# Optimization experiments

Measured on AMD Instinct MI355X. Metric: run time of the kernel, lower is better.

Reference implementation:

```python
import jax, jax.numpy as jnp
import numpy as np

B, S, D, H = 2, 2048, 1024, 16
HD = D // H  # head_dim = 64

def setup_inputs() -> dict:
    key = jax.random.key(0)
    ks = jax.random.split(key, 5)
    scale = 1.0 / np.sqrt(D)
    x = jax.random.normal(ks[0], (B, S, D), dtype=jnp.float32)
    Wq = jax.random.normal(ks[1], (D, D), dtype=jnp.float32) * scale
    Wk = jax.random.normal(ks[2], (D, D), dtype=jnp.float32) * scale
    Wv = jax.random.normal(ks[3], (D, D), dtype=jnp.float32) * scale
    Wf = jax.random.normal(ks[4], (D, D), dtype=jnp.float32) * scale
    z = jnp.zeros((D,), dtype=jnp.float32)
    return {"x": x, "Wq": Wq, "bq": z, "Wk": Wk, "bk": z, "Wv": Wv, "bv": z, "Wf": Wf, "bf": z}

def reference(x, Wq, bq, Wk, bk, Wv, bv, Wf, bf):
    # Linear layers follow torch convention: y = x @ W.T + b
    def split_heads(t):  # [B,S,D] -> [B,H,S,HD]
        return t.reshape(B, S, H, HD).transpose(0, 2, 1, 3)
    q = split_heads(x @ Wq.T + bq)
    k = split_heads(x @ Wk.T + bk)
    v = split_heads(x @ Wv.T + bv)
    scores = jnp.einsum('bhqd,bhkd->bhqk', q, k) / jnp.sqrt(jnp.float32(HD))
    causal = jnp.tril(jnp.ones((S, S), dtype=bool))  # [S,S]
    scores = jnp.where(causal[None, None], scores, -jnp.inf)
    attn = jax.nn.softmax(scores, axis=-1)
    out = jnp.einsum('bhqk,bhkd->bhqd', attn, v)
    out = out.transpose(0, 2, 1, 3).reshape(B, S, D)
    return out @ Wf.T + bf
```

## Files before the change

kernel.cpp:

```cpp
#include <hip/hip_runtime.h>
#include <stdint.h>

#define B_  2
#define S_  2048
#define D_  1024
#define H_  16
#define HD_ 64
#define M_  (B_*S_)

typedef __bf16 bf16x8 __attribute__((ext_vector_type(8)));
typedef float  f32x4  __attribute__((ext_vector_type(4)));

typedef const __attribute__((address_space(1))) void* gas_ptr;
typedef __attribute__((address_space(3))) void* las_ptr;

__device__ __forceinline__ uint16_t f32_to_bf16(float f) {
  uint32_t u = __float_as_uint(f);
  u += 0x7FFFu + ((u >> 16) & 1u);
  return (uint16_t)(u >> 16);
}

__device__ __forceinline__ uint16_t f32_to_bf16_rtz(float f) {
  return (uint16_t)(__float_as_uint(f) >> 16);
}

__device__ __forceinline__ void g2l16(const uint16_t* g, uint16_t* l) {
  __builtin_amdgcn_global_load_lds((gas_ptr)g, (las_ptr)l, 16, 0, 0);
}

__device__ __forceinline__ int swz_src(int s) {
  return (s >> 2) * D_ + (((s & 3) ^ ((s >> 3) & 3)) * 8);
}

__global__ void cast_all(const float* __restrict__ x,
                         const float* __restrict__ wq, const float* __restrict__ wk,
                         const float* __restrict__ wv, const float* __restrict__ wf,
                         uint16_t* __restrict__ xb,
                         uint16_t* __restrict__ wqb, uint16_t* __restrict__ wkb,
                         uint16_t* __restrict__ wvb, uint16_t* __restrict__ wfb) {
  const int X4 = M_ * D_ / 4;
  const int W4 = D_ * D_ / 4;
  int i = blockIdx.x * 256 + threadIdx.x;
  const float* src; uint16_t* dst; int off;
  if (i < X4) { src = x; dst = xb; off = i; }
  else {
    int j = i - X4;
    int w = j >> 18;
    off = j & (W4 - 1);
    src = (w == 0) ? wq : (w == 1) ? wk : (w == 2) ? wv : wf;
    dst = (w == 0) ? wqb : (w == 1) ? wkb : (w == 2) ? wvb : wfb;
  }
  float4 v = ((const float4*)src)[off];
  ushort4 o;
  o.x = f32_to_bf16(v.x); o.y = f32_to_bf16(v.y);
  o.z = f32_to_bf16(v.z); o.w = f32_to_bf16(v.w);
  ((ushort4*)dst)[off] = o;
}

__global__ __launch_bounds__(512, 2)
void qkv_gemm(const uint16_t* __restrict__ xb,
              const uint16_t* __restrict__ wqb, const uint16_t* __restrict__ wkb,
              const uint16_t* __restrict__ wvb,
              const float* __restrict__ bqv, const float* __restrict__ bkv,
              const float* __restrict__ bvv,
              uint16_t* __restrict__ qout, uint16_t* __restrict__ kout,
              uint16_t* __restrict__ vtout)
{
  __shared__ __align__(16) uint16_t As[2][2][8192];
  __shared__ __align__(16) uint16_t Bs[2][2][8192];

  const int wsel = blockIdx.x >> 2;
  const int nsel = blockIdx.x & 3;
  const int mtile = blockIdx.y;
  const int tid  = threadIdx.x;
  const int lane = tid & 63, wave = tid >> 6;
  const int quad = lane >> 4, l16 = lane & 15;
  const int wm = (wave >> 2) * 128;
  const int wn = (wave & 3) * 64;
  const int sw = quad ^ ((l16 >> 1) & 3);

  const uint16_t *Ap, *Bp;
  int m0e, n0e;
  if (wsel < 2) {
    Ap = xb; Bp = (wsel == 0) ? wqb : wkb;
    m0e = mtile * 256; n0e = nsel * 256;
  } else {
    Ap = wvb; Bp = xb;
    m0e = nsel * 256; n0e = mtile * 256;
  }

  const int so0 = swz_src(tid);
  const int so1 = swz_src(tid + 512);
  const uint16_t* gA = Ap + (size_t)m0e * D_;
  const uint16_t* gB = Bp + (size_t)n0e * D_;
  const int d0 = (wave * 64) * 8;
  const int d1 = (512 + wave * 64) * 8;

  f32x4 acc[8][4];
  #pragma unroll
  for (int i = 0; i < 8; ++i)
    #pragma unroll
    for (int j = 0; j < 4; ++j)
      #pragma unroll
      for (int e = 0; e < 4; ++e)
        acc[i][j][e] = 0.f;

  g2l16(gA + so0,      &As[0][0][d0]);
  g2l16(gA + 32 + so0, &As[0][1][d0]);
  g2l16(gB + so0,      &Bs[0][0][d0]);
  g2l16(gB + 32 + so0, &Bs[0][1][d0]);
  g2l16(gA + so1,      &As[0][0][d1]);
  g2l16(gA + 32 + so1, &As[0][1][d1]);
  g2l16(gB + so1,      &Bs[0][0][d1]);
  g2l16(gB + 32 + so1, &Bs[0][1][d1]);
  __syncthreads();

  bf16x8 bfr[4][2], afr[2][2];
  for (int t = 0; t < 16; ++t) {
    const int c = t & 1, cn = c ^ 1;
    const bool pf = (t < 15);
    const int kn = (t + 1) * 64;

    #pragma unroll
    for (int nt = 0; nt < 4; ++nt) {
      const int ro = ((wn + nt * 16 + l16) * 4 + sw) * 8;
      bfr[nt][0] = *(const bf16x8*)(&Bs[c][0][ro]);
      bfr[nt][1] = *(const bf16x8*)(&Bs[c][1][ro]);
    }

    #pragma unroll
    for (int p = 0; p < 4; ++p) {
      #pragma unroll
      for (int i = 0; i < 2; ++i) {
        const int ro = ((wm + (2 * p + i) * 16 + l16) * 4 + sw) * 8;
        afr[i][0] = *(const bf16x8*)(&As[c][0][ro]);
        afr[i][1] = *(const bf16x8*)(&As[c][1][ro]);
      }
      if (p == 0 && pf) {
        g2l16(gA + kn + so0,      &As[cn][0][d0]);
        g2l16(gA + kn + 32 + so0, &As[cn][1][d0]);
        g2l16(gB + kn + so0,      &Bs[cn][0][d0]);
        g2l16(gB + kn + 32 + so0, &Bs[cn][1][d0]);
      }
      if (p == 1 && pf) {
        g2l16(gA + kn + so1,      &As[cn][0][d1]);
        g2l16(gA + kn + 32 + so1, &As[cn][1][d1]);
        g2l16(gB + kn + so1,      &Bs[cn][0][d1]);
        g2l16(gB + kn + 32 + so1, &Bs[cn][1][d1]);
      }
      __builtin_amdgcn_s_barrier();
      asm volatile("s_waitcnt lgkmcnt(0)" ::: "memory");
      __builtin_amdgcn_sched_barrier(0);
      __builtin_amdgcn_s_setprio(1);
      #pragma unroll
      for (int i = 0; i < 2; ++i)
        #pragma unroll
        for (int nt = 0; nt < 4; ++nt) {
          acc[2 * p + i][nt] = __builtin_amdgcn_mfma_f32_16x16x32_bf16(
              afr[i][0], bfr[nt][0], acc[2 * p + i][nt], 0, 0, 0);
          acc[2 * p + i][nt] = __builtin_amdgcn_mfma_f32_16x16x32_bf16(
              afr[i][1], bfr[nt][1], acc[2 * p + i][nt], 0, 0, 0);
        }
      __builtin_amdgcn_s_setprio(0);
      if (p == 3) {
        asm volatile("s_waitcnt vmcnt(0)" ::: "memory");
      }
      __builtin_amdgcn_s_barrier();
    }
  }

  if (wsel < 2) {
    const float* bias = (wsel == 0) ? bqv : bkv;
    uint16_t* outp = (wsel == 0) ? qout : kout;
    const float scl = (wsel == 0) ? 0.18033688f : 1.0f;
    #pragma unroll
    for (int nt = 0; nt < 4; ++nt) {
      const int n = n0e + wn + nt * 16 + l16;
      const int h = n >> 6, hd = n & 63;
      const float bia = bias[n];
      #pragma unroll
      for (int mt = 0; mt < 8; ++mt) {
        #pragma unroll
        for (int r = 0; r < 4; ++r) {
          const int m = m0e + wm + mt * 16 + quad * 4 + r;
          const int bb = m >> 11, s = m & (S_ - 1);
          outp[(((size_t)(bb * H_ + h)) * S_ + s) * HD_ + hd] =
              f32_to_bf16((acc[mt][nt][r] + bia) * scl);
        }
      }
    }
  } else {
    #pragma unroll
    for (int mt = 0; mt < 8; ++mt) {
      #pragma unroll
      for (int r = 0; r < 4; ++r) {
        const int m = m0e + wm + mt * 16 + quad * 4 + r;
        const int h = m >> 6, hd = m & 63;
        const float bia = bvv[m];
        #pragma unroll
        for (int nt = 0; nt < 4; ++nt) {
          const int n = n0e + wn + nt * 16 + l16;
          const int bb = n >> 11, s = n & (S_ - 1);
          vtout[(((size_t)(bb * H_ + h)) * HD_ + hd) * S_ + s] =
              f32_to_bf16(acc[mt][nt][r] + bia);
        }
      }
    }
  }
}

__global__ __launch_bounds__(256)
void flash_attn(const uint16_t* __restrict__ qb, const uint16_t* __restrict__ kb,
                const uint16_t* __restrict__ vtb, uint16_t* __restrict__ ao)
{
  __shared__ __align__(16) uint16_t ks[2][64 * 32];
  __shared__ __align__(16) uint16_t vs[2][64 * 32];
  __shared__ __align__(16) uint16_t p_lds[4][16][72];

  const int bh = blockIdx.x;
  const int qt = (int)(gridDim.y - 1u - blockIdx.y);
  const int wave = threadIdx.x >> 6, lane = threadIdx.x & 63;
  const int quad = lane >> 4, l16 = lane & 15;
  const int sw = quad ^ ((l16 >> 1) & 3);
  const int q0 = qt * 64;

  const uint16_t* Q  = qb  + (size_t)bh * S_ * HD_;
  const uint16_t* Kp = kb  + (size_t)bh * S_ * HD_;
  const uint16_t* Vt = vtb + (size_t)bh * HD_ * S_;

  const int qrow = q0 + wave * 16;
  bf16x8 aq0 = *(const bf16x8*)(Q + (size_t)(qrow + l16) * HD_ + quad * 8);
  bf16x8 aq1 = *(const bf16x8*)(Q + (size_t)(qrow + l16) * HD_ + 32 + quad * 8);

  const int srow = lane >> 2;
  const int schk = (lane & 3) ^ ((lane >> 3) & 3);
  const uint16_t* sb[4]; uint16_t* sdst[4]; int sstep[4];
  #pragma unroll
  for (int j = 0; j < 4; ++j) {
    const int g = wave * 4 + j;
    if (g < 8) {
      const int c = (g >> 2) & 1, rb = g & 3;
      sdst[j] = &ks[c][rb * 512];
      sb[j] = Kp + (size_t)(rb * 16 + srow) * HD_ + c * 32 + schk * 8;
      sstep[j] = 64 * HD_;
    } else {
      const int gg = g - 8, c = (gg >> 2) & 1, rb = gg & 3;
      sdst[j] = &vs[c][rb * 512];
      sb[j] = Vt + (size_t)(rb * 16 + srow) * S_ + c * 32 + schk * 8;
      sstep[j] = 64;
    }
  }

  float lpart[4];
  f32x4 o[4];
  #pragma unroll
  for (int r = 0; r < 4; ++r) lpart[r] = 0.f;
  #pragma unroll
  for (int t = 0; t < 4; ++t)
    #pragma unroll
    for (int e = 0; e < 4; ++e) o[t][e] = 0.f;

  const int rowid = qrow + quad * 4;

  for (int kt = 0; kt <= qt; ++kt) {
    const int kbase = kt * 64;
    const bool diag = (kt == qt);

    #pragma unroll
    for (int j = 0; j < 4; ++j) {
      g2l16(sb[j], sdst[j]);
      sb[j] += sstep[j];
    }
    __syncthreads();

    bf16x8 kf0[4], kf1[4];
    #pragma unroll
    for (int nt = 0; nt < 4; ++nt) {
      kf0[nt] = *(const bf16x8*)(&ks[0][((nt * 16 + l16) * 4 + sw) * 8]);
      kf1[nt] = *(const bf16x8*)(&ks[1][((nt * 16 + l16) * 4 + sw) * 8]);
    }
    f32x4 sacc[4];
    #pragma unroll
    for (int nt = 0; nt < 4; ++nt) {
      #pragma unroll
      for (int e = 0; e < 4; ++e) sacc[nt][e] = 0.f;
      sacc[nt] = __builtin_amdgcn_mfma_f32_16x16x32_bf16(aq0, kf0[nt], sacc[nt], 0, 0, 0);
      sacc[nt] = __builtin_amdgcn_mfma_f32_16x16x32_bf16(aq1, kf1[nt], sacc[nt], 0, 0, 0);
    }

    bf16x8 vf0[4], vf1[4];
    #pragma unroll
    for (int t = 0; t < 4; ++t) {
      vf0[t] = *(const bf16x8*)(&vs[0][((t * 16 + l16) * 4 + sw) * 8]);
      vf1[t] = *(const bf16x8*)(&vs[1][((t * 16 + l16) * 4 + sw) * 8]);
    }

    #pragma unroll
    for (int nt = 0; nt < 4; ++nt) {
      const int kkc = kbase + nt * 16 + l16;
      #pragma unroll
      for (int r = 0; r < 4; ++r) {
        float p = __builtin_amdgcn_exp2f(sacc[nt][r]);
        if (diag && (kkc > rowid + r)) p = 0.f;
        lpart[r] += p;
        p_lds[wave][quad * 4 + r][nt * 16 + l16] = f32_to_bf16_rtz(p);
      }
    }

    bf16x8 ap0 = *(const bf16x8*)(&p_lds[wave][l16][quad * 8]);
    bf16x8 ap1 = *(const bf16x8*)(&p_lds[wave][l16][32 + quad * 8]);
    #pragma unroll
    for (int t = 0; t < 4; ++t) {
      o[t] = __builtin_amdgcn_mfma_f32_16x16x32_bf16(ap0, vf0[t], o[t], 0, 0, 0);
      o[t] = __builtin_amdgcn_mfma_f32_16x16x32_bf16(ap1, vf1[t], o[t], 0, 0, 0);
    }
    __syncthreads();
  }

  #pragma unroll
  for (int r = 0; r < 4; ++r) {
    lpart[r] += __shfl_xor(lpart[r], 1, 64);
    lpart[r] += __shfl_xor(lpart[r], 2, 64);
    lpart[r] += __shfl_xor(lpart[r], 4, 64);
    lpart[r] += __shfl_xor(lpart[r], 8, 64);
  }
  const int bb = bh >> 4, h = bh & 15;
  #pragma unroll
  for (int t = 0; t < 4; ++t) {
    #pragma unroll
    for (int r = 0; r < 4; ++r) {
      const float ov = o[t][r] / lpart[r];
      ao[((size_t)(bb * S_ + rowid + r)) * D_ + h * HD_ + t * 16 + l16] =
          f32_to_bf16(ov);
    }
  }
}

__global__ __launch_bounds__(256)
void out_gemm(const uint16_t* __restrict__ ab, const uint16_t* __restrict__ wfb,
              const float* __restrict__ bfv, float* __restrict__ out)
{
  __shared__ __align__(16) uint16_t As[2 * 64 * 32];
  __shared__ __align__(16) uint16_t Bs[2 * 128 * 32];
  const int m0 = blockIdx.y * 64;
  const int n0 = blockIdx.x * 128;
  const int lane = threadIdx.x & 63, wave = threadIdx.x >> 6;
  const int quad = lane >> 4, l16 = lane & 15;
  const int wm = (wave >> 1) * 32, wn = (wave & 1) * 64;
  const int sw = quad ^ ((l16 >> 1) & 3);

  f32x4 acc[2][4];
  #pragma unroll
  for (int i = 0; i < 2; ++i)
    #pragma unroll
    for (int j = 0; j < 4; ++j)
      #pragma unroll
      for (int e = 0; e < 4; ++e)
        acc[i][j][e] = 0.f;

  const int sA  = wave * 64 + lane;
  const int sB1 = sA + 256;
  const int soA = swz_src(sA), soB1 = swz_src(sB1);
  uint16_t* lA  = As + (size_t)(wave * 64) * 8;
  uint16_t* lB0 = Bs + (size_t)(wave * 64) * 8;
  uint16_t* lB1 = Bs + (size_t)(256 + wave * 64) * 8;
  const uint16_t* gA  = ab  + (size_t)m0 * D_ + soA;
  const uint16_t* gB0 = wfb + (size_t)n0 * D_ + soA;
  const uint16_t* gB1 = wfb + (size_t)n0 * D_ + soB1;

  for (int k0 = 0; k0 < D_; k0 += 64) {
    g2l16(gA  + k0,      lA);
    g2l16(gB0 + k0,      lB0);
    g2l16(gB1 + k0,      lB1);
    g2l16(gA  + k0 + 32, lA  + 2048);
    g2l16(gB0 + k0 + 32, lB0 + 4096);
    g2l16(gB1 + k0 + 32, lB1 + 4096);
    __syncthreads();
    bf16x8 af0[2], af1[2], bf0[4], bf1[4];
    #pragma unroll
    for (int mt = 0; mt < 2; ++mt) {
      const int ro = ((wm + mt * 16 + l16) * 4 + sw) * 8;
      af0[mt] = *(const bf16x8*)(As + ro);
      af1[mt] = *(const bf16x8*)(As + 2048 + ro);
    }
    #pragma unroll
    for (int nt = 0; nt < 4; ++nt) {
      const int ro = ((wn + nt * 16 + l16) * 4 + sw) * 8;
      bf0[nt] = *(const bf16x8*)(Bs + ro);
      bf1[nt] = *(const bf16x8*)(Bs + 4096 + ro);
    }
    #pragma unroll
    for (int mt = 0; mt < 2; ++mt)
      #pragma unroll
      for (int nt = 0; nt < 4; ++nt) {
        acc[mt][nt] = __builtin_amdgcn_mfma_f32_16x16x32_bf16(
            af0[mt], bf0[nt], acc[mt][nt], 0, 0, 0);
        acc[mt][nt] = __builtin_amdgcn_mfma_f32_16x16x32_bf16(
            af1[mt], bf1[nt], acc[mt][nt], 0, 0, 0);
      }
    __syncthreads();
  }

  #pragma unroll
  for (int nt = 0; nt < 4; ++nt) {
    const int n = n0 + wn + nt * 16 + l16;
    const float bia = bfv[n];
    #pragma unroll
    for (int mt = 0; mt < 2; ++mt) {
      #pragma unroll
      for (int r = 0; r < 4; ++r) {
        const int m = m0 + wm + mt * 16 + quad * 4 + r;
        out[(size_t)m * D_ + n] = acc[mt][nt][r] + bia;
      }
    }
  }
}

extern "C" void kernel_launch(void* const* d_in, const int* in_sizes, int n_in,
                              void* d_out, int out_size, void* d_ws, size_t ws_size,
                              hipStream_t stream) {
  (void)in_sizes; (void)n_in; (void)out_size; (void)ws_size;
  const float* x  = (const float*)d_in[0];
  const float* Wq = (const float*)d_in[1];
  const float* bq = (const float*)d_in[2];
  const float* Wk = (const float*)d_in[3];
  const float* bk = (const float*)d_in[4];
  const float* Wv = (const float*)d_in[5];
  const float* bv = (const float*)d_in[6];
  const float* Wf = (const float*)d_in[7];
  const float* bf = (const float*)d_in[8];
  float* out = (float*)d_out;

  uint16_t* ws = (uint16_t*)d_ws;
  uint16_t* xb   = ws;
  uint16_t* wqb  = xb  + (size_t)M_ * D_;
  uint16_t* wkb  = wqb + (size_t)D_ * D_;
  uint16_t* wvb  = wkb + (size_t)D_ * D_;
  uint16_t* wfb  = wvb + (size_t)D_ * D_;
  uint16_t* qbuf = wfb + (size_t)D_ * D_;
  uint16_t* kbuf = qbuf + (size_t)M_ * D_;
  uint16_t* vtb  = kbuf + (size_t)M_ * D_;
  uint16_t* aob  = vtb  + (size_t)M_ * D_;

  const int CAST_BLOCKS = (M_ * D_ / 4 + 4 * (D_ * D_ / 4)) / 256;
  cast_all<<<CAST_BLOCKS, 256, 0, stream>>>(x, Wq, Wk, Wv, Wf,
                                            xb, wqb, wkb, wvb, wfb);

  qkv_gemm<<<dim3(12, 16), 512, 0, stream>>>(xb, wqb, wkb, wvb, bq, bk, bv,
                                             qbuf, kbuf, vtb);
  flash_attn<<<dim3(32, 32), 256, 0, stream>>>(qbuf, kbuf, vtb, aob);
  out_gemm<<<dim3(8, 64), 256, 0, stream>>>(aob, wfb, bf, out);
}
```

Before: 181.4 us.

## Double-buffer K/V tiles in flash attention and split GEMM k-halves with partial waits

The flash attention kernel now keeps two K/V LDS buffers and prefetches the next key tile while computing the current one, so the global-to-LDS load and barrier no longer sit at the start of each iteration. MFMA blocks are wrapped in s_setprio. The projection GEMM restructures its inner loop by k-half, issuing each half's prefetch and using vmcnt partial waits so compute can start once the first half has landed. This doubles flash-attention LDS usage, which may reduce occupancy, and adds more barriers in the GEMM loop.

```diff
diff --git a/kernel.cpp b/kernel.cpp
--- a/kernel.cpp
+++ b/kernel.cpp
@@ -106,64 +106,73 @@
         acc[i][j][e] = 0.f;
 
   g2l16(gA + so0,      &As[0][0][d0]);
+  g2l16(gA + so1,      &As[0][0][d1]);
+  g2l16(gB + so0,      &Bs[0][0][d0]);
+  g2l16(gB + so1,      &Bs[0][0][d1]);
   g2l16(gA + 32 + so0, &As[0][1][d0]);
-  g2l16(gB + so0,      &Bs[0][0][d0]);
+  g2l16(gA + 32 + so1, &As[0][1][d1]);
   g2l16(gB + 32 + so0, &Bs[0][1][d0]);
-  g2l16(gA + so1,      &As[0][0][d1]);
-  g2l16(gA + 32 + so1, &As[0][1][d1]);
-  g2l16(gB + so1,      &Bs[0][0][d1]);
   g2l16(gB + 32 + so1, &Bs[0][1][d1]);
-  __syncthreads();
-
-  bf16x8 bfr[4][2], afr[2][2];
+  asm volatile("s_waitcnt vmcnt(4)" ::: "memory");
+  __builtin_amdgcn_s_barrier();
+
+  bf16x8 bfr[4], afr[4];
   for (int t = 0; t < 16; ++t) {
     const int c = t & 1, cn = c ^ 1;
     const bool pf = (t < 15);
     const int kn = (t + 1) * 64;
-
-    #pragma unroll
-    for (int nt = 0; nt < 4; ++nt) {
-      const int ro = ((wn + nt * 16 + l16) * 4 + sw) * 8;
-      bfr[nt][0] = *(const bf16x8*)(&Bs[c][0][ro]);
-      bfr[nt][1] = *(const bf16x8*)(&Bs[c][1][ro]);
-    }
-
-    #pragma unroll
-    for (int p = 0; p < 4; ++p) {
-      #pragma unroll
-      for (int i = 0; i < 2; ++i) {
-        const int ro = ((wm + (2 * p + i) * 16 + l16) * 4 + sw) * 8;
-        afr[i][0] = *(const bf16x8*)(&As[c][0][ro]);
-        afr[i][1] = *(const bf16x8*)(&As[c][1][ro]);
-      }
-      if (p == 0 && pf) {
-        g2l16(gA + kn + so0,      &As[cn][0][d0]);
-        g2l16(gA + kn + 32 + so0, &As[cn][1][d0]);
-        g2l16(gB + kn + so0,      &Bs[cn][0][d0]);
-        g2l16(gB + kn + 32 + so0, &Bs[cn][1][d0]);
-      }
-      if (p == 1 && pf) {
-        g2l16(gA + kn + so1,      &As[cn][0][d1]);
-        g2l16(gA + kn + 32 + so1, &As[cn][1][d1]);
-        g2l16(gB + kn + so1,      &Bs[cn][0][d1]);
-        g2l16(gB + kn + 32 + so1, &Bs[cn][1][d1]);
+    #pragma unroll
+    for (int h = 0; h < 2; ++h) {
+      #pragma unroll
+      for (int nt = 0; nt < 4; ++nt) {
+        const int ro = ((wn + nt * 16 + l16) * 4 + sw) * 8;
+        bfr[nt] = *(const bf16x8*)(&Bs[c][h][ro]);
+      }
+      #pragma unroll
+      for (int i = 0; i < 4; ++i) {
+        const int ro = ((wm + i * 16 + l16) * 4 + sw) * 8;
+        afr[i] = *(const bf16x8*)(&As[c][h][ro]);
+      }
+      if (pf) {
+        g2l16(gA + kn + h * 32 + so0, &As[cn][h][d0]);
+        g2l16(gA + kn + h * 32 + so1, &As[cn][h][d1]);
+        g2l16(gB + kn + h * 32 + so0, &Bs[cn][h][d0]);
+        g2l16(gB + kn + h * 32 + so1, &Bs[cn][h][d1]);
       }
       __builtin_amdgcn_s_barrier();
       asm volatile("s_waitcnt lgkmcnt(0)" ::: "memory");
       __builtin_amdgcn_sched_barrier(0);
       __builtin_amdgcn_s_setprio(1);
       #pragma unroll
-      for (int i = 0; i < 2; ++i)
+      for (int i = 0; i < 4; ++i)
         #pragma unroll
-        for (int nt = 0; nt < 4; ++nt) {
-          acc[2 * p + i][nt] = __builtin_amdgcn_mfma_f32_16x16x32_bf16(
-              afr[i][0], bfr[nt][0], acc[2 * p + i][nt], 0, 0, 0);
-          acc[2 * p + i][nt] = __builtin_amdgcn_mfma_f32_16x16x32_bf16(
-              afr[i][1], bfr[nt][1], acc[2 * p + i][nt], 0, 0, 0);
-        }
+        for (int nt = 0; nt < 4; ++nt)
+          acc[i][nt] = __builtin_amdgcn_mfma_f32_16x16x32_bf16(
+              afr[i], bfr[nt], acc[i][nt], 0, 0, 0);
       __builtin_amdgcn_s_setprio(0);
-      if (p == 3) {
-        asm volatile("s_waitcnt vmcnt(0)" ::: "memory");
+      __builtin_amdgcn_s_barrier();
+
+      #pragma unroll
+      for (int i = 0; i < 4; ++i) {
+        const int ro = ((wm + (4 + i) * 16 + l16) * 4 + sw) * 8;
+        afr[i] = *(const bf16x8*)(&As[c][h][ro]);
+      }
+      __builtin_amdgcn_s_barrier();
+      asm volatile("s_waitcnt lgkmcnt(0)" ::: "memory");
+      __builtin_amdgcn_sched_barrier(0);
+      __builtin_amdgcn_s_setprio(1);
+      #pragma unroll
+      for (int i = 0; i < 4; ++i)
+        #pragma unroll
+        for (int nt = 0; nt < 4; ++nt)
+          acc[4 + i][nt] = __builtin_amdgcn_mfma_f32_16x16x32_bf16(
+              afr[i], bfr[nt], acc[4 + i][nt], 0, 0, 0);
+      __builtin_amdgcn_s_setprio(0);
+      if (h == 0) {
+        if (pf) asm volatile("s_waitcnt vmcnt(8)" ::: "memory");
+        else    asm volatile("s_waitcnt vmcnt(0)" ::: "memory");
+      } else {
+        asm volatile("s_waitcnt vmcnt(4)" ::: "memory");
       }
       __builtin_amdgcn_s_barrier();
     }
@@ -213,8 +222,8 @@
 void flash_attn(const uint16_t* __restrict__ qb, const uint16_t* __restrict__ kb,
                 const uint16_t* __restrict__ vtb, uint16_t* __restrict__ ao)
 {
-  __shared__ __align__(16) uint16_t ks[2][64 * 32];
-  __shared__ __align__(16) uint16_t vs[2][64 * 32];
+  __shared__ __align__(16) uint16_t ks[2][2][2048];
+  __shared__ __align__(16) uint16_t vs[2][2][2048];
   __shared__ __align__(16) uint16_t p_lds[4][16][72];
 
   const int bh = blockIdx.x;
@@ -234,18 +243,20 @@
 
   const int srow = lane >> 2;
   const int schk = (lane & 3) ^ ((lane >> 3) & 3);
-  const uint16_t* sb[4]; uint16_t* sdst[4]; int sstep[4];
+  const uint16_t* sb[4]; uint16_t* sd0[4]; uint16_t* sd1[4]; int sstep[4];
   #pragma unroll
   for (int j = 0; j < 4; ++j) {
     const int g = wave * 4 + j;
     if (g < 8) {
       const int c = (g >> 2) & 1, rb = g & 3;
-      sdst[j] = &ks[c][rb * 512];
+      sd0[j] = &ks[0][c][rb * 512];
+      sd1[j] = &ks[1][c][rb * 512];
       sb[j] = Kp + (size_t)(rb * 16 + srow) * HD_ + c * 32 + schk * 8;
       sstep[j] = 64 * HD_;
     } else {
       const int gg = g - 8, c = (gg >> 2) & 1, rb = gg & 3;
-      sdst[j] = &vs[c][rb * 512];
+      sd0[j] = &vs[0][c][rb * 512];
+      sd1[j] = &vs[1][c][rb * 512];
       sb[j] = Vt + (size_t)(rb * 16 + srow) * S_ + c * 32 + schk * 8;
       sstep[j] = 64;
     }
@@ -261,25 +272,35 @@
     for (int e = 0; e < 4; ++e) o[t][e] = 0.f;
 
   const int rowid = qrow + quad * 4;
+
+  #pragma unroll
+  for (int j = 0; j < 4; ++j) {
+    g2l16(sb[j], sd0[j]);
+    sb[j] += sstep[j];
+  }
+  __syncthreads();
 
   for (int kt = 0; kt <= qt; ++kt) {
     const int kbase = kt * 64;
     const bool diag = (kt == qt);
-
-    #pragma unroll
-    for (int j = 0; j < 4; ++j) {
-      g2l16(sb[j], sdst[j]);
-      sb[j] += sstep[j];
-    }
-    __syncthreads();
+    const int cb = kt & 1;
+
+    if (kt < qt) {
+      #pragma unroll
+      for (int j = 0; j < 4; ++j) {
+        g2l16(sb[j], cb ? sd0[j] : sd1[j]);
+        sb[j] += sstep[j];
+      }
+    }
 
     bf16x8 kf0[4], kf1[4];
     #pragma unroll
     for (int nt = 0; nt < 4; ++nt) {
-      kf0[nt] = *(const bf16x8*)(&ks[0][((nt * 16 + l16) * 4 + sw) * 8]);
-      kf1[nt] = *(const bf16x8*)(&ks[1][((nt * 16 + l16) * 4 + sw) * 8]);
+      kf0[nt] = *(const bf16x8*)(&ks[cb][0][((nt * 16 + l16) * 4 + sw) * 8]);
+      kf1[nt] = *(const bf16x8*)(&ks[cb][1][((nt * 16 + l16) * 4 + sw) * 8]);
     }
     f32x4 sacc[4];
+    __builtin_amdgcn_s_setprio(1);
     #pragma unroll
     for (int nt = 0; nt < 4; ++nt) {
       #pragma unroll
@@ -287,12 +308,13 @@
       sacc[nt] = __builtin_amdgcn_mfma_f32_16x16x32_bf16(aq0, kf0[nt], sacc[nt], 0, 0, 0);
       sacc[nt] = __builtin_amdgcn_mfma_f32_16x16x32_bf16(aq1, kf1[nt], sacc[nt], 0, 0, 0);
     }
+    __builtin_amdgcn_s_setprio(0);
 
     bf16x8 vf0[4], vf1[4];
     #pragma unroll
     for (int t = 0; t < 4; ++t) {
-      vf0[t] = *(const bf16x8*)(&vs[0][((t * 16 + l16) * 4 + sw) * 8]);
-      vf1[t] = *(const bf16x8*)(&vs[1][((t * 16 + l16) * 4 + sw) * 8]);
+      vf0[t] = *(const bf16x8*)(&vs[cb][0][((t * 16 + l16) * 4 + sw) * 8]);
+      vf1[t] = *(const bf16x8*)(&vs[cb][1][((t * 16 + l16) * 4 + sw) * 8]);
     }
 
     #pragma unroll
@@ -309,11 +331,13 @@
 
     bf16x8 ap0 = *(const bf16x8*)(&p_lds[wave][l16][quad * 8]);
     bf16x8 ap1 = *(const bf16x8*)(&p_lds[wave][l16][32 + quad * 8]);
+    __builtin_amdgcn_s_setprio(1);
     #pragma unroll
     for (int t = 0; t < 4; ++t) {
       o[t] = __builtin_amdgcn_mfma_f32_16x16x32_bf16(ap0, vf0[t], o[t], 0, 0, 0);
       o[t] = __builtin_amdgcn_mfma_f32_16x16x32_bf16(ap1, vf1[t], o[t], 0, 0, 0);
     }
+    __builtin_amdgcn_s_setprio(0);
     __syncthreads();
   }
 
```

Result: no change. 181.5 us (+0.1%).
